# Kernel tuning notes

Hardware: AMD Instinct MI355X
Metric: run time of the kernel (lower is better)

The kernel has to match this reference:

```python
import jax, jax.numpy as jnp
import numpy as np

DIM = 256
EPS = 1e-8


def rmsnorm(y, scale):
    # full RMSNorm (p < 0): rms = ||y||_2 / sqrt(d)
    norm = jnp.linalg.norm(y, axis=-1, keepdims=True)
    rms = norm * (DIM ** -0.5)
    return scale * (y / (rms + EPS))


def setup_inputs() -> dict:
    key = jax.random.key(0)
    ks = jax.random.split(key, 12)
    d = DIM
    inp = {
        "agent": jax.random.normal(ks[0], (64, d), dtype=jnp.float32),
        "x": jax.random.normal(ks[1], (8, 8192, d), dtype=jnp.float32),
        "W_qkv": jax.random.normal(ks[2], (3 * d, d), dtype=jnp.float32) * 0.02,
        "b_qkv": jnp.zeros((3 * d,), dtype=jnp.float32),
        "W_agent": jax.random.normal(ks[3], (2 * d, d), dtype=jnp.float32) * 0.02,
        "b_agent": jnp.zeros((2 * d,), dtype=jnp.float32),
        "W_fc1": jax.random.normal(ks[4], (d, d), dtype=jnp.float32) * 0.02,
        "b_fc1": jnp.zeros((d,), dtype=jnp.float32),
        "W_fc2": jax.random.normal(ks[5], (d, d), dtype=jnp.float32) * 0.02,
        "b_fc2": jnp.zeros((d,), dtype=jnp.float32),
        "norm_scale": jnp.ones((d,), dtype=jnp.float32),
    }
    return inp


def reference(agent, x, W_qkv, b_qkv, W_agent, b_agent, W_fc1, b_fc1, W_fc2, b_fc2, norm_scale):
    sc = DIM ** -0.5
    # qkv projection of x: [B, N, 3d] -> q, k, v each [B, N, d]
    qkv = x @ W_qkv.T + b_qkv
    q, k, v = jnp.split(qkv, 3, axis=-1)
    # agent projection: [K, 2d] -> q_agent, k_agent each [K, d]
    qa_ka = agent @ W_agent.T + b_agent
    q_agent, k_agent = jnp.split(qa_ka, 2, axis=-1)
    # stage 1: agents attend over tokens  -> [B, K, N]
    attn1 = jax.nn.softmax(jnp.einsum('kd,bnd->bkn', q_agent, k) * sc, axis=-1)
    v1 = jnp.einsum('bkn,bnd->bkd', attn1, v)  # [B, K, d]
    v1 = v1 @ W_fc1.T + b_fc1
    # stage 2: tokens attend over agents -> [B, N, K]
    attn2 = jax.nn.softmax(jnp.einsum('bnd,kd->bnk', q, k_agent) * sc, axis=-1)
    v2 = jnp.einsum('bnk,bkd->bnd', attn2, v1)  # [B, N, d]
    v2 = v2 @ W_fc2.T + b_fc2
    return rmsnorm(v2 + x, norm_scale)
```

## Files before the change

kernel.cpp:

```cpp
#include <hip/hip_runtime.h>
#include <hip/hip_bf16.h>

typedef __attribute__((ext_vector_type(4))) float f32x4;
typedef __attribute__((ext_vector_type(8))) short s16x8;
typedef __attribute__((ext_vector_type(4))) short s16x4;

__device__ __forceinline__ unsigned short f2bf(float f) {
    unsigned int u; __builtin_memcpy(&u, &f, 4);
    u += 0x7fffu + ((u >> 16) & 1u);
    return (unsigned short)(u >> 16);
}
__device__ __forceinline__ float bf2f(unsigned short h) {
    unsigned int u = ((unsigned int)h) << 16;
    float f; __builtin_memcpy(&f, &u, 4);
    return f;
}
__device__ __forceinline__ s16x8 pack8(f32x4 a, f32x4 b) {
    s16x8 r;
    r[0] = (short)f2bf(a[0]); r[1] = (short)f2bf(a[1]);
    r[2] = (short)f2bf(a[2]); r[3] = (short)f2bf(a[3]);
    r[4] = (short)f2bf(b[0]); r[5] = (short)f2bf(b[1]);
    r[6] = (short)f2bf(b[2]); r[7] = (short)f2bf(b[3]);
    return r;
}

template<bool AF32, bool BF32, bool OUTBF16, bool BIAS>
__global__ __launch_bounds__(256) void gemm_k256(
    const void* __restrict__ Ap, long sA, long bAstr,
    const void* __restrict__ Bp, long sB,
    const float* __restrict__ bias,
    void* __restrict__ Cp, long sC, long bCstr,
    int M, int N)
{
    __shared__ alignas(16) unsigned short As[128 * 256];
    __shared__ alignas(16) unsigned short Bs[64 * 256];
    const int tid = threadIdx.x;
    const int lane = tid & 63;
    const int w = tid >> 6;
    const int m0 = blockIdx.x * 128;
    const int nt = blockIdx.y;
    const int z = blockIdx.z;

    {
        const int kk = (tid & 31) * 8;
        #pragma unroll
        for (int j = 0; j < 16; ++j) {
            const int row = (tid >> 5) + j * 8;
            int rowg = m0 + row; if (rowg > M - 1) rowg = M - 1;
            s16x8 v;
            if constexpr (AF32) {
                const float* s = (const float*)Ap + (size_t)z * bAstr + (size_t)rowg * sA + kk;
                f32x4 f0 = *(const f32x4*)s;
                f32x4 f1 = *(const f32x4*)(s + 4);
                v = pack8(f0, f1);
            } else {
                const unsigned short* s = (const unsigned short*)Ap + (size_t)z * bAstr + (size_t)rowg * sA + kk;
                v = *(const s16x8*)s;
            }
            *(s16x8*)((char*)As + row * 512 + ((kk * 2) ^ ((row & 7) << 4))) = v;
        }
        #pragma unroll
        for (int j = 0; j < 8; ++j) {
            const int row = (tid >> 5) + j * 8;
            const int rowg = nt * 64 + row;
            s16x8 v;
            if constexpr (BF32) {
                const float* s = (const float*)Bp + (size_t)rowg * sB + kk;
                f32x4 f0 = *(const f32x4*)s;
                f32x4 f1 = *(const f32x4*)(s + 4);
                v = pack8(f0, f1);
            } else {
                const unsigned short* s = (const unsigned short*)Bp + (size_t)rowg * sB + kk;
                v = *(const s16x8*)s;
            }
            *(s16x8*)((char*)Bs + row * 512 + ((kk * 2) ^ ((row & 7) << 4))) = v;
        }
    }
    __syncthreads();

    f32x4 acc[2][4];
    const f32x4 zero = {0.f, 0.f, 0.f, 0.f};
    #pragma unroll
    for (int rf = 0; rf < 2; ++rf)
        #pragma unroll
        for (int cf = 0; cf < 4; ++cf)
            acc[rf][cf] = zero;

    #pragma unroll
    for (int ks = 0; ks < 8; ++ks) {
        const int kb = ks * 64 + ((lane >> 4) << 4);
        s16x8 areg[2], bfr[4];
        #pragma unroll
        for (int rf = 0; rf < 2; ++rf) {
            const int row = w * 32 + rf * 16 + (lane & 15);
            areg[rf] = *(const s16x8*)((const char*)As + row * 512 + (kb ^ ((row & 7) << 4)));
        }
        #pragma unroll
        for (int cf = 0; cf < 4; ++cf) {
            const int row = cf * 16 + (lane & 15);
            bfr[cf] = *(const s16x8*)((const char*)Bs + row * 512 + (kb ^ ((row & 7) << 4)));
        }
        #pragma unroll
        for (int rf = 0; rf < 2; ++rf)
            #pragma unroll
            for (int cf = 0; cf < 4; ++cf)
                acc[rf][cf] = __builtin_amdgcn_mfma_f32_16x16x32_bf16(
                    areg[rf], bfr[cf], acc[rf][cf], 0, 0, 0);
    }

    #pragma unroll
    for (int cf = 0; cf < 4; ++cf) {
        const int n = nt * 64 + cf * 16 + (lane & 15);
        const float bv = BIAS ? bias[n] : 0.f;
        #pragma unroll
        for (int rf = 0; rf < 2; ++rf) {
            #pragma unroll
            for (int r = 0; r < 4; ++r) {
                const int m = m0 + w * 32 + rf * 16 + ((lane >> 4) << 2) + r;
                if (m < M) {
                    const float v = acc[rf][cf][r] + bv;
                    const size_t co = (size_t)z * bCstr + (size_t)m * sC + n;
                    if constexpr (OUTBF16) ((unsigned short*)Cp)[co] = f2bf(v);
                    else                   ((float*)Cp)[co] = v;
                }
            }
        }
    }
}

__global__ __launch_bounds__(256) void build_M2(
    const float* __restrict__ W_qkv, const float* __restrict__ b_qkv,
    const float* __restrict__ qa_out,
    unsigned short* __restrict__ MS, float* __restrict__ cbias)
{
    const int i = blockIdx.x;
    const int t = threadIdx.x;
    __shared__ float qs[256];
    const int a = i & 63;
    const bool isS1 = (i < 64);
    qs[t] = qa_out[(size_t)a * 512 + (isS1 ? t : 256 + t)] * 0.0625f;
    __syncthreads();
    const float* W  = W_qkv + (isS1 ? 256 * 256 : 0);
    const float* bb = b_qkv + (isS1 ? 256 : 0);
    float acc = 0.f, cb = 0.f;
    for (int dout = 0; dout < 256; ++dout) {
        const float q = qs[dout];
        acc += q * W[(size_t)dout * 256 + t];
        cb  += q * bb[dout];
    }
    MS[i * 256 + t] = f2bf(acc);
    if (t == 0) cbias[i] = cb;
}

__global__ __launch_bounds__(256) void xproj2(
    const float* __restrict__ x,
    const unsigned short* __restrict__ MS,
    const float* __restrict__ cbias,
    float* __restrict__ S1T,
    float* __restrict__ S2,
    float* __restrict__ mpart, float* __restrict__ lpart)
{
    __shared__ alignas(16) unsigned short As[64 * 256];
    const int tid = threadIdx.x, lane = tid & 63, w = tid >> 6;
    const int lr = lane & 15, lq = lane >> 4;
    const long m0 = (long)blockIdx.x * 64;

    {
        const int k0 = (tid & 31) * 8;
        #pragma unroll
        for (int j = 0; j < 8; ++j) {
            const int row = (tid >> 5) + j * 8;
            const float* s = x + (m0 + row) * 256 + k0;
            f32x4 f0 = *(const f32x4*)s;
            f32x4 f1 = *(const f32x4*)(s + 4);
            *(s16x8*)((char*)As + row * 512 + ((k0 * 2) ^ ((row & 7) << 4))) = pack8(f0, f1);
        }
    }
    __syncthreads();

    f32x4 acc[4][2];
    const f32x4 zero = {0.f, 0.f, 0.f, 0.f};
    #pragma unroll
    for (int rf = 0; rf < 4; ++rf)
        #pragma unroll
        for (int j = 0; j < 2; ++j)
            acc[rf][j] = zero;

    #pragma unroll
    for (int ks = 0; ks < 8; ++ks) {
        const int kb = ks * 64 + lq * 16;
        s16x8 areg[4];
        #pragma unroll
        for (int rf = 0; rf < 4; ++rf) {
            const int row = rf * 16 + lr;
            areg[rf] = *(const s16x8*)((const char*)As + row * 512 + (kb ^ ((row & 7) << 4)));
        }
        s16x8 bfr[2];
        #pragma unroll
        for (int j = 0; j < 2; ++j) {
            const int msrow = j * 64 + w * 16 + lr;
            bfr[j] = *(const s16x8*)((const char*)MS + (size_t)msrow * 512 + kb);
        }
        #pragma unroll
        for (int rf = 0; rf < 4; ++rf)
            #pragma unroll
            for (int j = 0; j < 2; ++j)
                acc[rf][j] = __builtin_amdgcn_mfma_f32_16x16x32_bf16(
                    areg[rf], bfr[j], acc[rf][j], 0, 0, 0);
    }

    #pragma unroll
    for (int j = 0; j < 2; ++j) {
        const int a = w * 16 + lr;
        const float bv = cbias[j * 64 + a];
        float* dst = j ? S2 : S1T;
        float mx = -1e30f;
        #pragma unroll
        for (int rf = 0; rf < 4; ++rf)
            #pragma unroll
            for (int r = 0; r < 4; ++r) {
                const float v = acc[rf][j][r] + bv;
                dst[(m0 + rf * 16 + lq * 4 + r) * 64 + a] = v;
                mx = fmaxf(mx, v);
            }
        if (j == 0) {
            mx = fmaxf(mx, __shfl_xor(mx, 16));
            mx = fmaxf(mx, __shfl_xor(mx, 32));
            float sm = 0.f;
            #pragma unroll
            for (int rf = 0; rf < 4; ++rf)
                #pragma unroll
                for (int r = 0; r < 4; ++r)
                    sm += __expf(acc[rf][j][r] + bv - mx);
            sm += __shfl_xor(sm, 16);
            sm += __shfl_xor(sm, 32);
            if (lq == 0) {
                mpart[(size_t)blockIdx.x * 64 + a] = mx;
                lpart[(size_t)blockIdx.x * 64 + a] = sm;
            }
        }
    }
}

__global__ __launch_bounds__(256) void s1_combine(const float* __restrict__ mpart,
                                                  const float* __restrict__ lpart,
                                                  float* __restrict__ m1,
                                                  float* __restrict__ l1inv)
{
    const int b = blockIdx.x;
    const int a = threadIdx.x & 63, s = threadIdx.x >> 6;
    float M = -1e30f;
    for (int c = s; c < 128; c += 4)
        M = fmaxf(M, mpart[((size_t)b * 128 + c) * 64 + a]);
    float L = 0.f;
    for (int c = s; c < 128; c += 4) {
        const size_t idx = ((size_t)b * 128 + c) * 64 + a;
        L += lpart[idx] * __expf(mpart[idx] - M);
    }
    __shared__ float ms[256], ls[256];
    ms[threadIdx.x] = M; ls[threadIdx.x] = L;
    __syncthreads();
    if (threadIdx.x < 64) {
        const int aa = threadIdx.x;
        float Mm = ms[aa];
        #pragma unroll
        for (int ss = 1; ss < 4; ++ss) Mm = fmaxf(Mm, ms[ss * 64 + aa]);
        float Ll = 0.f;
        #pragma unroll
        for (int ss = 0; ss < 4; ++ss) Ll += ls[ss * 64 + aa] * __expf(ms[ss * 64 + aa] - Mm);
        m1[b * 64 + aa] = Mm;
        l1inv[b * 64 + aa] = 1.0f / Ll;
    }
}

__global__ __launch_bounds__(256) void pv_mfma2(
    const float* __restrict__ S1T,
    const float* __restrict__ x,
    const float* __restrict__ m1,
    const float* __restrict__ l1inv,
    float* __restrict__ y_part)
{
    __shared__ alignas(16) unsigned short P_lds[64 * 128];
    __shared__ alignas(16) unsigned short XT[128 * 136];
    const int tid = threadIdx.x, lane = tid & 63, w = tid >> 6;
    const int lr = lane & 15, lq = lane >> 4;
    const int c = blockIdx.x, dh = blockIdx.y, b = blockIdx.z;

    const int a4 = (tid & 15) * 4;
    const f32x4 m4 = *(const f32x4*)&m1[b * 64 + a4];
    const f32x4 l4 = *(const f32x4*)&l1inv[b * 64 + a4];

    f32x4 acc[4][2];
    const f32x4 zero = {0.f, 0.f, 0.f, 0.f};
    #pragma unroll
    for (int rf = 0; rf < 4; ++rf)
        #pragma unroll
        for (int cf = 0; cf < 2; ++cf)
            acc[rf][cf] = zero;

    for (int kt = 0; kt < 2; ++kt) {
        const size_t ng0 = (size_t)b * 8192 + c * 256 + kt * 128;
        #pragma unroll
        for (int pass = 0; pass < 4; ++pass) {
            const int np = 2 * (tid >> 4) + pass * 32;
            const float* s = S1T + (ng0 + np) * 64 + a4;
            f32x4 s0 = *(const f32x4*)s;
            f32x4 s1 = *(const f32x4*)(s + 64);
            #pragma unroll
            for (int j = 0; j < 4; ++j) {
                const int a = a4 + j;
                const float p0 = __expf(s0[j] - m4[j]) * l4[j];
                const float p1 = __expf(s1[j] - m4[j]) * l4[j];
                const unsigned int pk = (unsigned int)f2bf(p0) | ((unsigned int)f2bf(p1) << 16);
                *(unsigned int*)((char*)P_lds + a * 256 + ((np * 2) ^ (((a >> 1) & 7) << 4))) = pk;
            }
        }
        {
            const int nh = tid >> 2;
            const int dq = tid & 3;
            const float* xbase = x + (ng0 + 2 * nh) * 256 + dh * 128;
            #pragma unroll
            for (int pass = 0; pass < 8; ++pass) {
                const int dl0 = pass * 16 + dq * 4;
                f32x4 xa = *(const f32x4*)(xbase + dl0);
                f32x4 xb = *(const f32x4*)(xbase + 256 + dl0);
                #pragma unroll
                for (int jj = 0; jj < 4; ++jj) {
                    const unsigned int pk = (unsigned int)f2bf(xa[jj]) | ((unsigned int)f2bf(xb[jj]) << 16);
                    *(unsigned int*)((char*)XT + (dl0 + jj) * 272 + nh * 4) = pk;
                }
            }
        }
        __syncthreads();
        #pragma unroll
        for (int ks = 0; ks < 4; ++ks) {
            const int kbn = ks * 64 + lq * 16;
            s16x8 af[4], bfv[2];
            #pragma unroll
            for (int rf = 0; rf < 4; ++rf) {
                const int row = rf * 16 + lr;
                af[rf] = *(const s16x8*)((const char*)P_lds + row * 256 + (kbn ^ (((row >> 1) & 7) << 4)));
            }
            #pragma unroll
            for (int cf = 0; cf < 2; ++cf) {
                const int dl = w * 32 + cf * 16 + lr;
                bfv[cf] = *(const s16x8*)((const char*)XT + dl * 272 + kbn);
            }
            #pragma unroll
            for (int rf = 0; rf < 4; ++rf)
                #pragma unroll
                for (int cf = 0; cf < 2; ++cf)
                    acc[rf][cf] = __builtin_amdgcn_mfma_f32_16x16x32_bf16(
                        af[rf], bfv[cf], acc[rf][cf], 0, 0, 0);
        }
        __syncthreads();
    }
    #pragma unroll
    for (int rf = 0; rf < 4; ++rf)
        #pragma unroll
        for (int cf = 0; cf < 2; ++cf)
            #pragma unroll
            for (int r = 0; r < 4; ++r) {
                const int a = rf * 16 + lq * 4 + r;
                const int d = dh * 128 + w * 32 + cf * 16 + lr;
                y_part[(((size_t)b * 32 + c) * 64 + a) * 256 + d] = acc[rf][cf][r];
            }
}

__global__ void v1_reduce(const float* __restrict__ y_part,
                          float* __restrict__ y_raw)
{
    const int a = blockIdx.x, b = blockIdx.y, t = threadIdx.x;
    f32x4 s = {0.f, 0.f, 0.f, 0.f};
    for (int c = 0; c < 32; ++c)
        s += *(const f32x4*)&y_part[(((size_t)b * 32 + c) * 64 + a) * 256 + t * 4];
    *(f32x4*)&y_raw[((size_t)b * 64 + a) * 256 + t * 4] = s;
}

__global__ __launch_bounds__(256) void stage2_final(const float* __restrict__ S2,
                                                    const float* __restrict__ uu,
                                                    const float* __restrict__ x,
                                                    const float* __restrict__ nscale,
                                                    float* __restrict__ out)
{
    __shared__ alignas(16) unsigned short uT[256 * 64];
    __shared__ alignas(16) unsigned short P[64 * 64];
    __shared__ float ssq[4][64];
    const int tid = threadIdx.x, lane = tid & 63, w = tid >> 6;
    const int lr = lane & 15, lq = lane >> 4;
    const int b = blockIdx.x >> 7;
    const long n0 = (long)blockIdx.x * 64;

    {
        const int pr = tid >> 3;
        const int sub = tid & 7;
        const float* u0 = uu + ((size_t)b * 64 + 2 * pr) * 256;
        #pragma unroll
        for (int pass = 0; pass < 8; ++pass) {
            const int d0 = pass * 32 + sub * 4;
            f32x4 ua = *(const f32x4*)(u0 + d0);
            f32x4 ub = *(const f32x4*)(u0 + 256 + d0);
            #pragma unroll
            for (int jj = 0; jj < 4; ++jj) {
                const int d = d0 + jj;
                const unsigned int pk = (unsigned int)f2bf(ua[jj]) | ((unsigned int)f2bf(ub[jj]) << 16);
                *(unsigned int*)((char*)uT + d * 128 + ((pr * 4) ^ ((d & 7) << 4))) = pk;
            }
        }
    }
    {
        const int t = lane >> 2, q = lane & 3;
        const int nl = w * 16 + t;
        const float* srow = S2 + (n0 + nl) * 64 + q * 16;
        f32x4 sv[4];
        #pragma unroll
        for (int j = 0; j < 4; ++j) sv[j] = *(const f32x4*)(srow + j * 4);
        float mx = -1e30f;
        #pragma unroll
        for (int j = 0; j < 4; ++j)
            #pragma unroll
            for (int e = 0; e < 4; ++e) mx = fmaxf(mx, sv[j][e]);
        mx = fmaxf(mx, __shfl_xor(mx, 1));
        mx = fmaxf(mx, __shfl_xor(mx, 2));
        float p[16];
        float sm = 0.f;
        #pragma unroll
        for (int j = 0; j < 4; ++j)
            #pragma unroll
            for (int e = 0; e < 4; ++e) {
                p[j * 4 + e] = __expf(sv[j][e] - mx);
                sm += p[j * 4 + e];
            }
        sm += __shfl_xor(sm, 1);
        sm += __shfl_xor(sm, 2);
        const float rs = 1.f / sm;
        s16x8 o0, o1;
        #pragma unroll
        for (int e = 0; e < 8; ++e) o0[e] = (short)f2bf(p[e] * rs);
        #pragma unroll
        for (int e = 0; e < 8; ++e) o1[e] = (short)f2bf(p[8 + e] * rs);
        const int swz = (nl & 7) << 4;
        *(s16x8*)((char*)P + nl * 128 + ((q * 32) ^ swz)) = o0;
        *(s16x8*)((char*)P + nl * 128 + ((q * 32 + 16) ^ swz)) = o1;
    }
    __syncthreads();

    f32x4 acc[4][4];
    const f32x4 zero = {0.f, 0.f, 0.f, 0.f};
    #pragma unroll
    for (int rf = 0; rf < 4; ++rf)
        #pragma unroll
        for (int cf = 0; cf < 4; ++cf)
            acc[rf][cf] = zero;
    #pragma unroll
    for (int ks = 0; ks < 2; ++ks) {
        const int kb = ks * 64 + lq * 16;
        s16x8 af[4], bfv[4];
        #pragma unroll
        for (int rf = 0; rf < 4; ++rf) {
            const int dR = w * 64 + rf * 16 + lr;
            af[rf] = *(const s16x8*)((const char*)uT + dR * 128 + (kb ^ ((dR & 7) << 4)));
        }
        #pragma unroll
        for (int cf = 0; cf < 4; ++cf) {
            const int nR = cf * 16 + lr;
            bfv[cf] = *(const s16x8*)((const char*)P + nR * 128 + (kb ^ ((nR & 7) << 4)));
        }
        #pragma unroll
        for (int rf = 0; rf < 4; ++rf)
            #pragma unroll
            for (int cf = 0; cf < 4; ++cf)
                acc[rf][cf] = __builtin_amdgcn_mfma_f32_16x16x32_bf16(
                    af[rf], bfv[cf], acc[rf][cf], 0, 0, 0);
    }

    float part[4] = {0.f, 0.f, 0.f, 0.f};
    #pragma unroll
    for (int cf = 0; cf < 4; ++cf) {
        const long n = n0 + cf * 16 + lr;
        #pragma unroll
        for (int rf = 0; rf < 4; ++rf) {
            const int d0 = w * 64 + rf * 16 + lq * 4;
            const f32x4 xr = *(const f32x4*)&x[n * 256 + d0];
            acc[rf][cf] += xr;
            part[cf] += acc[rf][cf][0] * acc[rf][cf][0] + acc[rf][cf][1] * acc[rf][cf][1]
                      + acc[rf][cf][2] * acc[rf][cf][2] + acc[rf][cf][3] * acc[rf][cf][3];
        }
    }
    #pragma unroll
    for (int cf = 0; cf < 4; ++cf) {
        float s = part[cf];
        s += __shfl_xor(s, 16);
        s += __shfl_xor(s, 32);
        if (lq == 0) ssq[w][cf * 16 + lr] = s;
    }
    __syncthreads();

    #pragma unroll
    for (int cf = 0; cf < 4; ++cf) {
        const int tokl = cf * 16 + lr;
        const float tot = ssq[0][tokl] + ssq[1][tokl] + ssq[2][tokl] + ssq[3][tokl];
        const float inv = 1.f / (sqrtf(tot) * 0.0625f + 1e-8f);
        const long n = n0 + tokl;
        #pragma unroll
        for (int rf = 0; rf < 4; ++rf) {
            const int d0 = w * 64 + rf * 16 + lq * 4;
            const f32x4 sc4 = *(const f32x4*)&nscale[d0];
            f32x4 o = sc4 * acc[rf][cf] * inv;
            *(f32x4*)&out[n * 256 + d0] = o;
        }
    }
}

extern "C" void kernel_launch(void* const* d_in, const int* in_sizes, int n_in,
                              void* d_out, int out_size, void* d_ws, size_t ws_size,
                              hipStream_t stream)
{
    const float* agent   = (const float*)d_in[0];
    const float* x       = (const float*)d_in[1];
    const float* W_qkv   = (const float*)d_in[2];
    const float* b_qkv   = (const float*)d_in[3];
    const float* W_agent = (const float*)d_in[4];
    const float* b_agent = (const float*)d_in[5];
    const float* W_fc1   = (const float*)d_in[6];
    const float* b_fc1   = (const float*)d_in[7];
    const float* W_fc2   = (const float*)d_in[8];
    const float* b_fc2   = (const float*)d_in[9];
    const float* nscale  = (const float*)d_in[10];
    float* out = (float*)d_out;

    char* wsp = (char*)d_ws;
    size_t off = 0;
    auto alloc = [&](size_t n) { void* p = wsp + off; off += (n + 255) & ~(size_t)255; return p; };

    float*  qa_out = (float*)alloc(64UL * 512 * 4);
    unsigned short* MS = (unsigned short*)alloc(128UL * 256 * 2);
    float*  cbias  = (float*)alloc(128UL * 4);
    float*  S1T    = (float*)alloc(65536UL * 64 * 4);
    float*  S2     = (float*)alloc(65536UL * 64 * 4);
    float*  mpart  = (float*)alloc(1024UL * 64 * 4);
    float*  lpart  = (float*)alloc(1024UL * 64 * 4);
    float*  m1     = (float*)alloc(512UL * 4);
    float*  l1inv  = (float*)alloc(512UL * 4);
    float*  y_part = (float*)alloc(8UL * 32 * 64 * 256 * 4);
    float*  y_raw  = (float*)alloc(512UL * 256 * 4);
    float*  t0     = (float*)alloc(512UL * 256 * 4);
    float*  t1     = (float*)alloc(512UL * 256 * 4);
    float*  uu     = (float*)alloc(512UL * 256 * 4);

    gemm_k256<true, true, false, true><<<dim3(1, 8, 1), 256, 0, stream>>>(
        agent, 256, 0, W_agent, 256, b_agent, qa_out, 512, 0, 64, 512);
    build_M2<<<128, 256, 0, stream>>>(W_qkv, b_qkv, qa_out, MS, cbias);
    xproj2<<<1024, 256, 0, stream>>>(x, MS, cbias, S1T, S2, mpart, lpart);
    s1_combine<<<8, 256, 0, stream>>>(mpart, lpart, m1, l1inv);
    pv_mfma2<<<dim3(32, 2, 8), 256, 0, stream>>>(S1T, x, m1, l1inv, y_part);
    v1_reduce<<<dim3(64, 8), 64, 0, stream>>>(y_part, y_raw);
    gemm_k256<true, true, false, true><<<dim3(4, 4, 1), 256, 0, stream>>>(
        y_raw, 256, 0, W_qkv + 512 * 256, 256, b_qkv + 512, t0, 256, 0, 512, 256);
    gemm_k256<true, true, false, true><<<dim3(4, 4, 1), 256, 0, stream>>>(
        t0, 256, 0, W_fc1, 256, b_fc1, t1, 256, 0, 512, 256);
    gemm_k256<true, true, false, true><<<dim3(4, 4, 1), 256, 0, stream>>>(
        t1, 256, 0, W_fc2, 256, b_fc2, uu, 256, 0, 512, 256);
    stage2_final<<<1024, 256, 0, stream>>>(S2, uu, x, nscale, out);
}
```

Baseline: 140.5 us.

## Fuse stage-2 softmax into xproj2 and store bf16 probabilities

The stage-2 row softmax over agents moves into the projection kernel. The MFMA work for the second half is remapped so each wave holds complete token rows across all 64 agents, letting the softmax finish with in-wave shuffles. It then writes swizzled bf16 probabilities instead of fp32 logits, which halves the intermediate buffer and removes the exp/normalize work from stage2_final, now a plain copy into LDS. The cost is scattered 2-byte global stores and extra LDS reads of the A fragments in xproj2.

Result: slower. 149.5 us (+6.4%).

```diff
diff --git a/kernel.cpp b/kernel.cpp
--- a/kernel.cpp
+++ b/kernel.cpp
@@ -157,7 +157,7 @@
     const unsigned short* __restrict__ MS,
     const float* __restrict__ cbias,
     float* __restrict__ S1T,
-    float* __restrict__ S2,
+    unsigned short* __restrict__ P2,
     float* __restrict__ mpart, float* __restrict__ lpart)
 {
     __shared__ alignas(16) unsigned short As[64 * 256];
@@ -178,14 +178,13 @@
     }
     __syncthreads();
 
-    f32x4 acc[4][2];
+    f32x4 acc0[4];
+    f32x4 acc1[4];
     const f32x4 zero = {0.f, 0.f, 0.f, 0.f};
     #pragma unroll
-    for (int rf = 0; rf < 4; ++rf)
-        #pragma unroll
-        for (int j = 0; j < 2; ++j)
-            acc[rf][j] = zero;
-
+    for (int i = 0; i < 4; ++i) { acc0[i] = zero; acc1[i] = zero; }
+
+    const int roww = w * 16 + lr;
     #pragma unroll
     for (int ks = 0; ks < 8; ++ks) {
         const int kb = ks * 64 + lq * 16;
@@ -195,49 +194,76 @@
             const int row = rf * 16 + lr;
             areg[rf] = *(const s16x8*)((const char*)As + row * 512 + (kb ^ ((row & 7) << 4)));
         }
-        s16x8 bfr[2];
-        #pragma unroll
-        for (int j = 0; j < 2; ++j) {
-            const int msrow = j * 64 + w * 16 + lr;
-            bfr[j] = *(const s16x8*)((const char*)MS + (size_t)msrow * 512 + kb);
-        }
+        s16x8 b0 = *(const s16x8*)((const char*)MS + (size_t)(w * 16 + lr) * 512 + kb);
         #pragma unroll
         for (int rf = 0; rf < 4; ++rf)
-            #pragma unroll
-            for (int j = 0; j < 2; ++j)
-                acc[rf][j] = __builtin_amdgcn_mfma_f32_16x16x32_bf16(
-                    areg[rf], bfr[j], acc[rf][j], 0, 0, 0);
-    }
-
-    #pragma unroll
-    for (int j = 0; j < 2; ++j) {
+            acc0[rf] = __builtin_amdgcn_mfma_f32_16x16x32_bf16(areg[rf], b0, acc0[rf], 0, 0, 0);
+        s16x8 aw = *(const s16x8*)((const char*)As + roww * 512 + (kb ^ ((roww & 7) << 4)));
+        s16x8 b1[4];
+        #pragma unroll
+        for (int cf = 0; cf < 4; ++cf)
+            b1[cf] = *(const s16x8*)((const char*)MS + (size_t)(64 + cf * 16 + lr) * 512 + kb);
+        #pragma unroll
+        for (int cf = 0; cf < 4; ++cf)
+            acc1[cf] = __builtin_amdgcn_mfma_f32_16x16x32_bf16(aw, b1[cf], acc1[cf], 0, 0, 0);
+    }
+
+    {
         const int a = w * 16 + lr;
-        const float bv = cbias[j * 64 + a];
-        float* dst = j ? S2 : S1T;
+        const float bv = cbias[a];
         float mx = -1e30f;
         #pragma unroll
         for (int rf = 0; rf < 4; ++rf)
             #pragma unroll
             for (int r = 0; r < 4; ++r) {
-                const float v = acc[rf][j][r] + bv;
-                dst[(m0 + rf * 16 + lq * 4 + r) * 64 + a] = v;
+                const float v = acc0[rf][r] + bv;
+                S1T[(m0 + rf * 16 + lq * 4 + r) * 64 + a] = v;
                 mx = fmaxf(mx, v);
             }
-        if (j == 0) {
-            mx = fmaxf(mx, __shfl_xor(mx, 16));
-            mx = fmaxf(mx, __shfl_xor(mx, 32));
-            float sm = 0.f;
-            #pragma unroll
-            for (int rf = 0; rf < 4; ++rf)
-                #pragma unroll
-                for (int r = 0; r < 4; ++r)
-                    sm += __expf(acc[rf][j][r] + bv - mx);
-            sm += __shfl_xor(sm, 16);
-            sm += __shfl_xor(sm, 32);
-            if (lq == 0) {
-                mpart[(size_t)blockIdx.x * 64 + a] = mx;
-                lpart[(size_t)blockIdx.x * 64 + a] = sm;
-            }
+        mx = fmaxf(mx, __shfl_xor(mx, 16));
+        mx = fmaxf(mx, __shfl_xor(mx, 32));
+        float sm = 0.f;
+        #pragma unroll
+        for (int rf = 0; rf < 4; ++rf)
+            #pragma unroll
+            for (int r = 0; r < 4; ++r)
+                sm += __expf(acc0[rf][r] + bv - mx);
+        sm += __shfl_xor(sm, 16);
+        sm += __shfl_xor(sm, 32);
+        if (lq == 0) {
+            mpart[(size_t)blockIdx.x * 64 + a] = mx;
+            lpart[(size_t)blockIdx.x * 64 + a] = sm;
+        }
+    }
+
+    {
+        float bv1[4];
+        #pragma unroll
+        for (int cf = 0; cf < 4; ++cf) bv1[cf] = cbias[64 + cf * 16 + lr];
+        #pragma unroll
+        for (int r = 0; r < 4; ++r) {
+            float v[4];
+            #pragma unroll
+            for (int cf = 0; cf < 4; ++cf) v[cf] = acc1[cf][r] + bv1[cf];
+            float m = fmaxf(fmaxf(v[0], v[1]), fmaxf(v[2], v[3]));
+            m = fmaxf(m, __shfl_xor(m, 1));
+            m = fmaxf(m, __shfl_xor(m, 2));
+            m = fmaxf(m, __shfl_xor(m, 4));
+            m = fmaxf(m, __shfl_xor(m, 8));
+            float p[4], s = 0.f;
+            #pragma unroll
+            for (int cf = 0; cf < 4; ++cf) { p[cf] = __expf(v[cf] - m); s += p[cf]; }
+            s += __shfl_xor(s, 1);
+            s += __shfl_xor(s, 2);
+            s += __shfl_xor(s, 4);
+            s += __shfl_xor(s, 8);
+            const float rs = 1.f / s;
+            const int nl = w * 16 + lq * 4 + r;
+            const int swz = (nl & 7) << 4;
+            char* row = (char*)P2 + (m0 + nl) * 128;
+            #pragma unroll
+            for (int cf = 0; cf < 4; ++cf)
+                *(unsigned short*)(row + ((2 * (cf * 16 + lr)) ^ swz)) = f2bf(p[cf] * rs);
         }
     }
 }
@@ -377,7 +403,7 @@
     *(f32x4*)&y_raw[((size_t)b * 64 + a) * 256 + t * 4] = s;
 }
 
-__global__ __launch_bounds__(256) void stage2_final(const float* __restrict__ S2,
+__global__ __launch_bounds__(256) void stage2_final(const unsigned short* __restrict__ P2,
                                                     const float* __restrict__ uu,
                                                     const float* __restrict__ x,
                                                     const float* __restrict__ nscale,
@@ -409,39 +435,12 @@
         }
     }
     {
-        const int t = lane >> 2, q = lane & 3;
-        const int nl = w * 16 + t;
-        const float* srow = S2 + (n0 + nl) * 64 + q * 16;
-        f32x4 sv[4];
-        #pragma unroll
-        for (int j = 0; j < 4; ++j) sv[j] = *(const f32x4*)(srow + j * 4);
-        float mx = -1e30f;
-        #pragma unroll
-        for (int j = 0; j < 4; ++j)
-            #pragma unroll
-            for (int e = 0; e < 4; ++e) mx = fmaxf(mx, sv[j][e]);
-        mx = fmaxf(mx, __shfl_xor(mx, 1));
-        mx = fmaxf(mx, __shfl_xor(mx, 2));
-        float p[16];
-        float sm = 0.f;
-        #pragma unroll
-        for (int j = 0; j < 4; ++j)
-            #pragma unroll
-            for (int e = 0; e < 4; ++e) {
-                p[j * 4 + e] = __expf(sv[j][e] - mx);
-                sm += p[j * 4 + e];
-            }
-        sm += __shfl_xor(sm, 1);
-        sm += __shfl_xor(sm, 2);
-        const float rs = 1.f / sm;
-        s16x8 o0, o1;
-        #pragma unroll
-        for (int e = 0; e < 8; ++e) o0[e] = (short)f2bf(p[e] * rs);
-        #pragma unroll
-        for (int e = 0; e < 8; ++e) o1[e] = (short)f2bf(p[8 + e] * rs);
-        const int swz = (nl & 7) << 4;
-        *(s16x8*)((char*)P + nl * 128 + ((q * 32) ^ swz)) = o0;
-        *(s16x8*)((char*)P + nl * 128 + ((q * 32 + 16) ^ swz)) = o1;
+        const int row = tid & 63, seg = tid >> 6;
+        const char* src = (const char*)P2 + (n0 + row) * 128 + seg * 32;
+        s16x8 v0 = *(const s16x8*)src;
+        s16x8 v1 = *(const s16x8*)(src + 16);
+        *(s16x8*)((char*)P + row * 128 + seg * 32) = v0;
+        *(s16x8*)((char*)P + row * 128 + seg * 32 + 16) = v1;
     }
     __syncthreads();
 
@@ -537,7 +536,7 @@
     unsigned short* MS = (unsigned short*)alloc(128UL * 256 * 2);
     float*  cbias  = (float*)alloc(128UL * 4);
     float*  S1T    = (float*)alloc(65536UL * 64 * 4);
-    float*  S2     = (float*)alloc(65536UL * 64 * 4);
+    unsigned short* P2 = (unsigned short*)alloc(65536UL * 64 * 2);
     float*  mpart  = (float*)alloc(1024UL * 64 * 4);
     float*  lpart  = (float*)alloc(1024UL * 64 * 4);
     float*  m1     = (float*)alloc(512UL * 4);
@@ -551,7 +550,7 @@
     gemm_k256<true, true, false, true><<<dim3(1, 8, 1), 256, 0, stream>>>(
         agent, 256, 0, W_agent, 256, b_agent, qa_out, 512, 0, 64, 512);
     build_M2<<<128, 256, 0, stream>>>(W_qkv, b_qkv, qa_out, MS, cbias);
-    xproj2<<<1024, 256, 0, stream>>>(x, MS, cbias, S1T, S2, mpart, lpart);
+    xproj2<<<1024, 256, 0, stream>>>(x, MS, cbias, S1T, P2, mpart, lpart);
     s1_combine<<<8, 256, 0, stream>>>(mpart, lpart, m1, l1inv);
     pv_mfma2<<<dim3(32, 2, 8), 256, 0, stream>>>(S1T, x, m1, l1inv, y_part);
     v1_reduce<<<dim3(64, 8), 64, 0, stream>>>(y_part, y_raw);
@@ -561,5 +560,5 @@
         t0, 256, 0, W_fc1, 256, b_fc1, t1, 256, 0, 512, 256);
     gemm_k256<true, true, false, true><<<dim3(4, 4, 1), 256, 0, stream>>>(
         t1, 256, 0, W_fc2, 256, b_fc2, uu, 256, 0, 512, 256);
-    stage2_final<<<1024, 256, 0, stream>>>(S2, uu, x, nscale, out);
-}
+    stage2_final<<<1024, 256, 0, stream>>>(P2, uu, x, nscale, out);
+}
```

## Fuse agent projection and softmax combine into consumers, chain GEMMs in bf16

Applied to the files above, without the earlier changes.

Folds the agent projection GEMM into build_M2, so each block computes its own q_agent/k_agent row, and folds the s1_combine reduction into the prologue of pv_mfma2, which removes two kernel launches. The intermediate v1 chain (y_raw, t0, t1) is now stored as bf16, with the GEMM template flags switched to bf16 inputs and outputs, halving those buffers. In exchange, every pv_mfma2 block redundantly re-reduces the 128 softmax partials, and the extra bf16 rounding in the small GEMM chain costs some precision.

Result: faster. 135.6 us (-3.5%).

```diff
diff --git a/kernel.cpp b/kernel.cpp
--- a/kernel.cpp
+++ b/kernel.cpp
@@ -130,15 +130,29 @@
 
 __global__ __launch_bounds__(256) void build_M2(
     const float* __restrict__ W_qkv, const float* __restrict__ b_qkv,
-    const float* __restrict__ qa_out,
+    const float* __restrict__ agent, const float* __restrict__ W_agent,
+    const float* __restrict__ b_agent,
     unsigned short* __restrict__ MS, float* __restrict__ cbias)
 {
     const int i = blockIdx.x;
     const int t = threadIdx.x;
+    __shared__ float ag[256];
     __shared__ float qs[256];
     const int a = i & 63;
     const bool isS1 = (i < 64);
-    qs[t] = qa_out[(size_t)a * 512 + (isS1 ? t : 256 + t)] * 0.0625f;
+    ag[t] = agent[(size_t)a * 256 + t];
+    __syncthreads();
+    const int tp = isS1 ? t : 256 + t;
+    {
+        const float* wr = W_agent + (size_t)tp * 256;
+        float q = 0.f;
+        #pragma unroll 4
+        for (int d = 0; d < 256; d += 4) {
+            f32x4 wv = *(const f32x4*)(wr + d);
+            q += ag[d] * wv[0] + ag[d + 1] * wv[1] + ag[d + 2] * wv[2] + ag[d + 3] * wv[3];
+        }
+        qs[t] = (q + b_agent[tp]) * 0.0625f;
+    }
     __syncthreads();
     const float* W  = W_qkv + (isS1 ? 256 * 256 : 0);
     const float* bb = b_qkv + (isS1 ? 256 : 0);
@@ -242,42 +256,11 @@
     }
 }
 
-__global__ __launch_bounds__(256) void s1_combine(const float* __restrict__ mpart,
-                                                  const float* __restrict__ lpart,
-                                                  float* __restrict__ m1,
-                                                  float* __restrict__ l1inv)
-{
-    const int b = blockIdx.x;
-    const int a = threadIdx.x & 63, s = threadIdx.x >> 6;
-    float M = -1e30f;
-    for (int c = s; c < 128; c += 4)
-        M = fmaxf(M, mpart[((size_t)b * 128 + c) * 64 + a]);
-    float L = 0.f;
-    for (int c = s; c < 128; c += 4) {
-        const size_t idx = ((size_t)b * 128 + c) * 64 + a;
-        L += lpart[idx] * __expf(mpart[idx] - M);
-    }
-    __shared__ float ms[256], ls[256];
-    ms[threadIdx.x] = M; ls[threadIdx.x] = L;
-    __syncthreads();
-    if (threadIdx.x < 64) {
-        const int aa = threadIdx.x;
-        float Mm = ms[aa];
-        #pragma unroll
-        for (int ss = 1; ss < 4; ++ss) Mm = fmaxf(Mm, ms[ss * 64 + aa]);
-        float Ll = 0.f;
-        #pragma unroll
-        for (int ss = 0; ss < 4; ++ss) Ll += ls[ss * 64 + aa] * __expf(ms[ss * 64 + aa] - Mm);
-        m1[b * 64 + aa] = Mm;
-        l1inv[b * 64 + aa] = 1.0f / Ll;
-    }
-}
-
 __global__ __launch_bounds__(256) void pv_mfma2(
     const float* __restrict__ S1T,
     const float* __restrict__ x,
-    const float* __restrict__ m1,
-    const float* __restrict__ l1inv,
+    const float* __restrict__ mpart,
+    const float* __restrict__ lpart,
     float* __restrict__ y_part)
 {
     __shared__ alignas(16) unsigned short P_lds[64 * 128];
@@ -285,10 +268,43 @@
     const int tid = threadIdx.x, lane = tid & 63, w = tid >> 6;
     const int lr = lane & 15, lq = lane >> 4;
     const int c = blockIdx.x, dh = blockIdx.y, b = blockIdx.z;
-
     const int a4 = (tid & 15) * 4;
-    const f32x4 m4 = *(const f32x4*)&m1[b * 64 + a4];
-    const f32x4 l4 = *(const f32x4*)&l1inv[b * 64 + a4];
+
+    f32x4 m4, l4;
+    {
+        float* scratch = (float*)XT;
+        const int a = tid & 63, s4 = tid >> 6;
+        const size_t bb = (size_t)b * 128;
+        float M = -1e30f;
+        for (int cc = s4; cc < 128; cc += 4)
+            M = fmaxf(M, mpart[(bb + cc) * 64 + a]);
+        float L = 0.f;
+        for (int cc = s4; cc < 128; cc += 4) {
+            const size_t idx = (bb + cc) * 64 + a;
+            L += lpart[idx] * __expf(mpart[idx] - M);
+        }
+        scratch[tid] = M;
+        scratch[256 + tid] = L;
+        __syncthreads();
+        if (tid < 64) {
+            float Mm = scratch[tid];
+            #pragma unroll
+            for (int ss = 1; ss < 4; ++ss) Mm = fmaxf(Mm, scratch[ss * 64 + tid]);
+            float Ll = 0.f;
+            #pragma unroll
+            for (int ss = 0; ss < 4; ++ss)
+                Ll += scratch[256 + ss * 64 + tid] * __expf(scratch[ss * 64 + tid] - Mm);
+            scratch[512 + tid] = Mm;
+            scratch[576 + tid] = 1.0f / Ll;
+        }
+        __syncthreads();
+        #pragma unroll
+        for (int j = 0; j < 4; ++j) {
+            m4[j] = scratch[512 + a4 + j];
+            l4[j] = scratch[576 + a4 + j];
+        }
+        __syncthreads();
+    }
 
     f32x4 acc[4][2];
     const f32x4 zero = {0.f, 0.f, 0.f, 0.f};
@@ -368,13 +384,16 @@
 }
 
 __global__ void v1_reduce(const float* __restrict__ y_part,
-                          float* __restrict__ y_raw)
+                          unsigned short* __restrict__ y_rawb)
 {
     const int a = blockIdx.x, b = blockIdx.y, t = threadIdx.x;
     f32x4 s = {0.f, 0.f, 0.f, 0.f};
     for (int c = 0; c < 32; ++c)
         s += *(const f32x4*)&y_part[(((size_t)b * 32 + c) * 64 + a) * 256 + t * 4];
-    *(f32x4*)&y_raw[((size_t)b * 64 + a) * 256 + t * 4] = s;
+    s16x4 pk;
+    #pragma unroll
+    for (int j = 0; j < 4; ++j) pk[j] = (short)f2bf(s[j]);
+    *(s16x4*)&y_rawb[((size_t)b * 64 + a) * 256 + t * 4] = pk;
 }
 
 __global__ __launch_bounds__(256) void stage2_final(const float* __restrict__ S2,
@@ -533,33 +552,27 @@
     size_t off = 0;
     auto alloc = [&](size_t n) { void* p = wsp + off; off += (n + 255) & ~(size_t)255; return p; };
 
-    float*  qa_out = (float*)alloc(64UL * 512 * 4);
     unsigned short* MS = (unsigned short*)alloc(128UL * 256 * 2);
     float*  cbias  = (float*)alloc(128UL * 4);
     float*  S1T    = (float*)alloc(65536UL * 64 * 4);
     float*  S2     = (float*)alloc(65536UL * 64 * 4);
     float*  mpart  = (float*)alloc(1024UL * 64 * 4);
     float*  lpart  = (float*)alloc(1024UL * 64 * 4);
-    float*  m1     = (float*)alloc(512UL * 4);
-    float*  l1inv  = (float*)alloc(512UL * 4);
     float*  y_part = (float*)alloc(8UL * 32 * 64 * 256 * 4);
-    float*  y_raw  = (float*)alloc(512UL * 256 * 4);
-    float*  t0     = (float*)alloc(512UL * 256 * 4);
-    float*  t1     = (float*)alloc(512UL * 256 * 4);
+    unsigned short* y_rawb = (unsigned short*)alloc(512UL * 256 * 2);
+    unsigned short* t0b    = (unsigned short*)alloc(512UL * 256 * 2);
+    unsigned short* t1b    = (unsigned short*)alloc(512UL * 256 * 2);
     float*  uu     = (float*)alloc(512UL * 256 * 4);
 
-    gemm_k256<true, true, false, true><<<dim3(1, 8, 1), 256, 0, stream>>>(
-        agent, 256, 0, W_agent, 256, b_agent, qa_out, 512, 0, 64, 512);
-    build_M2<<<128, 256, 0, stream>>>(W_qkv, b_qkv, qa_out, MS, cbias);
+    build_M2<<<128, 256, 0, stream>>>(W_qkv, b_qkv, agent, W_agent, b_agent, MS, cbias);
     xproj2<<<1024, 256, 0, stream>>>(x, MS, cbias, S1T, S2, mpart, lpart);
-    s1_combine<<<8, 256, 0, stream>>>(mpart, lpart, m1, l1inv);
-    pv_mfma2<<<dim3(32, 2, 8), 256, 0, stream>>>(S1T, x, m1, l1inv, y_part);
-    v1_reduce<<<dim3(64, 8), 64, 0, stream>>>(y_part, y_raw);
-    gemm_k256<true, true, false, true><<<dim3(4, 4, 1), 256, 0, stream>>>(
-        y_raw, 256, 0, W_qkv + 512 * 256, 256, b_qkv + 512, t0, 256, 0, 512, 256);
-    gemm_k256<true, true, false, true><<<dim3(4, 4, 1), 256, 0, stream>>>(
-        t0, 256, 0, W_fc1, 256, b_fc1, t1, 256, 0, 512, 256);
-    gemm_k256<true, true, false, true><<<dim3(4, 4, 1), 256, 0, stream>>>(
-        t1, 256, 0, W_fc2, 256, b_fc2, uu, 256, 0, 512, 256);
+    pv_mfma2<<<dim3(32, 2, 8), 256, 0, stream>>>(S1T, x, mpart, lpart, y_part);
+    v1_reduce<<<dim3(64, 8), 64, 0, stream>>>(y_part, y_rawb);
+    gemm_k256<false, true, true, true><<<dim3(4, 4, 1), 256, 0, stream>>>(
+        y_rawb, 256, 0, W_qkv + 512 * 256, 256, b_qkv + 512, t0b, 256, 0, 512, 256);
+    gemm_k256<false, true, true, true><<<dim3(4, 4, 1), 256, 0, stream>>>(
+        t0b, 256, 0, W_fc1, 256, b_fc1, t1b, 256, 0, 512, 256);
+    gemm_k256<false, true, false, true><<<dim3(4, 4, 1), 256, 0, stream>>>(
+        t1b, 256, 0, W_fc2, 256, b_fc2, uu, 256, 0, 512, 256);
     stage2_final<<<1024, 256, 0, stream>>>(S2, uu, x, nscale, out);
 }
```
